# Optimization experiments

Hardware: AMD Instinct MI355X
Metric: run time of the kernel (lower is better)

Reference implementation:

```python
import jax, jax.numpy as jnp
import numpy as np

B, T, D_IN, H, D_DEC = 64, 512, 512, 1024, 1024


def _lstm_scan(xs, W_ih, W_hh, b_ih, b_hh):
    """xs: (T, B, D). Returns hs: (T, B, H), final (h, c). Zero initial state,
    matching torch.nn.LSTMCell default when no state is passed."""
    Bsz = xs.shape[1]
    Hsz = W_hh.shape[1]
    h0 = jnp.zeros((Bsz, Hsz), xs.dtype)
    c0 = jnp.zeros((Bsz, Hsz), xs.dtype)

    def step(carry, x):
        h, c = carry
        # gates: (B, 4H), torch order [i, f, g, o]
        g = x @ W_ih.T + b_ih + h @ W_hh.T + b_hh
        i, f, gg, o = jnp.split(g, 4, axis=-1)
        c_new = jax.nn.sigmoid(f) * c + jax.nn.sigmoid(i) * jnp.tanh(gg)
        h_new = jax.nn.sigmoid(o) * jnp.tanh(c_new)
        return (h_new, c_new), h_new

    (hT, cT), hs = jax.lax.scan(step, (h0, c0), xs)
    return hs, hT, cT


def setup_inputs() -> dict:
    key = jax.random.key(0)
    ks = jax.random.split(key, 14)
    s_cell = 1.0 / np.sqrt(H)
    s_fc = 1.0 / np.sqrt(2 * H)
    u = lambda k, shape, s: jax.random.uniform(k, shape, jnp.float32, -s, s)
    return {
        "embedding_input": jax.random.normal(ks[0], (B, T, D_IN), jnp.float32),
        "W_ih_f": u(ks[1], (4 * H, D_IN), s_cell),
        "W_hh_f": u(ks[2], (4 * H, H), s_cell),
        "b_ih_f": u(ks[3], (4 * H,), s_cell),
        "b_hh_f": u(ks[4], (4 * H,), s_cell),
        "W_ih_b": u(ks[5], (4 * H, D_IN), s_cell),
        "W_hh_b": u(ks[6], (4 * H, H), s_cell),
        "b_ih_b": u(ks[7], (4 * H,), s_cell),
        "b_hh_b": u(ks[8], (4 * H,), s_cell),
        "fc_W": u(ks[9], (D_DEC, 2 * H), s_fc),
        "fc_b": u(ks[10], (D_DEC,), s_fc),
        "fh_W": u(ks[11], (D_DEC, 2 * H), s_fc),
        "fh_b": u(ks[12], (D_DEC,), s_fc),
    }


def reference(embedding_input, W_ih_f, W_hh_f, b_ih_f, b_hh_f,
              W_ih_b, W_hh_b, b_ih_b, b_hh_b, fc_W, fc_b, fh_W, fh_b):
    xs = jnp.transpose(embedding_input, (1, 0, 2))  # (T, B, D)
    # forward direction over t = 0..T-1
    hs_f, hT_f, cT_f = _lstm_scan(xs, W_ih_f, W_hh_f, b_ih_f, b_hh_f)
    # backward direction over t = T-1..0; torch code stores these in
    # traversal order (NOT flipped back), so we keep that order.
    hs_b, hT_b, cT_b = _lstm_scan(xs[::-1], W_ih_b, W_hh_b, b_ih_b, b_hh_b)

    cell_end = jnp.concatenate([cT_f, cT_b], axis=-1)     # (B, 2H)
    hidden_end = jnp.concatenate([hT_f, hT_b], axis=-1)   # (B, 2H)
    initial_cells = jnp.tanh(cell_end @ fc_W.T + fc_b)
    initial_hiddens = jnp.tanh(hidden_end @ fh_W.T + fh_b)

    # (B, T, 2H): forward slot t = timestep t; backward slot t = timestep T-1-t
    hidden_states = jnp.concatenate([hs_f, hs_b], axis=-1).transpose(1, 0, 2)
    return hidden_states, (initial_hiddens, initial_cells)
```

## Files before the change

### kernel.cpp

```cpp
#include <hip/hip_runtime.h>
#include <stdint.h>
#include <math.h>


#define TSEQ 512
#define DIN  512

typedef short  short8  __attribute__((ext_vector_type(8)));
typedef float  float4_ __attribute__((ext_vector_type(4)));
typedef float  float8_ __attribute__((ext_vector_type(8)));

__device__ __forceinline__ unsigned short f2bf(float f) {
  union { float f; unsigned int i; } v; v.f = f;
  unsigned int r = (v.i + 0x7FFFu + ((v.i >> 16) & 1u)) >> 16;
  return (unsigned short)r;
}
__device__ __forceinline__ short8 cvt8(const float* p) {
  float8_ f = *reinterpret_cast<const float8_*>(p);
  short8 s;
  #pragma unroll
  for (int i = 0; i < 8; ++i) s[i] = (short)f2bf(f[i]);
  return s;
}
__device__ __forceinline__ short8 ald16(const unsigned long long* b64, size_t elem) {
  union { unsigned long long u[2]; short8 s; } v;
  const unsigned long long* p = b64 + (elem >> 2);
  v.u[0] = __hip_atomic_load(p,     __ATOMIC_RELAXED, __HIP_MEMORY_SCOPE_AGENT);
  v.u[1] = __hip_atomic_load(p + 1, __ATOMIC_RELAXED, __HIP_MEMORY_SCOPE_AGENT);
  return v.s;
}
__device__ __forceinline__ float sigf(float x) {
  x = fminf(fmaxf(x, -30.f), 30.f);
  return 1.f / (1.f + expf(-x));
}

__global__ __launch_bounds__(512, 2)
void lstm_encoder_kernel(
    const float* __restrict__ x,
    const float* __restrict__ Wih_f, const float* __restrict__ Whh_f,
    const float* __restrict__ bih_f, const float* __restrict__ bhh_f,
    const float* __restrict__ Wih_b, const float* __restrict__ Whh_b,
    const float* __restrict__ bih_b, const float* __restrict__ bhh_b,
    const float* __restrict__ fcW, const float* __restrict__ fcb,
    const float* __restrict__ fhW, const float* __restrict__ fhb,
    float* __restrict__ out,
    unsigned char* __restrict__ flags, int* __restrict__ done,
    unsigned short* __restrict__ hbuf_f, unsigned short* __restrict__ hbuf_b,
    unsigned short* __restrict__ cend)
{
  __shared__ float part[8][4][32][18];

  const int tid  = threadIdx.x;
  const int wv   = tid >> 6;
  const int lane = tid & 63;
  const int quad = lane >> 4;
  const int u16  = lane & 15;

  const int wg    = blockIdx.x;
  const int group = wg >> 7;
  const int rem   = wg & 127;
  const int dir   = rem >> 6;
  const int seg   = rem & 63;
  const int j0    = seg * 16;
  const int dom   = group * 2 + dir;
  unsigned char* myflags = flags + dom * 256;

  const float* Wih = dir ? Wih_b : Wih_f;
  const float* Whh = dir ? Whh_b : Whh_f;
  const float* bih = dir ? bih_b : bih_f;
  const float* bhh = dir ? bhh_b : bhh_f;
  unsigned short* hbuf = dir ? hbuf_b : hbuf_f;
  const unsigned long long* hbuf64 = (const unsigned long long*)hbuf;
  unsigned int* hbuf32 = (unsigned int*)hbuf;

  const int wx = wv * 64;
  const int wh = wv * 128;

  short8 Bf[6][4];
  #pragma unroll
  for (int kc = 0; kc < 6; ++kc) {
    #pragma unroll
    for (int nt = 0; nt < 4; ++nt) {
      const int row = nt * 1024 + j0 + u16;
      const float* p = (kc < 2)
          ? (Wih + (size_t)row * 512  + (wx + kc * 32 + quad * 8))
          : (Whh + (size_t)row * 1024 + (wh + (kc - 2) * 32 + quad * 8));
      Bf[kc][nt] = cvt8(p);
    }
  }
  float bias[4];
  #pragma unroll
  for (int g = 0; g < 4; ++g)
    bias[g] = bih[g * 1024 + j0 + u16] + bhh[g * 1024 + j0 + u16];

  float4_ acc[2][4];
  #pragma unroll
  for (int mt = 0; mt < 2; ++mt)
    #pragma unroll
    for (int nt = 0; nt < 4; ++nt) acc[mt][nt] = (float4_){0.f, 0.f, 0.f, 0.f};

  float cstate = 0.f;
  const int arow0 = group * 32 + u16;

  auto gemm_x = [&](int t) {
    const int tx = dir ? (TSEQ - 1 - t) : t;
    #pragma unroll
    for (int kc = 0; kc < 2; ++kc) {
      const int klane = wx + kc * 32 + quad * 8;
      const float* base = x + ((size_t)arow0 * TSEQ + tx) * DIN + klane;
      short8 a0 = cvt8(base);
      short8 a1 = cvt8(base + (size_t)16 * TSEQ * DIN);
      #pragma unroll
      for (int nt = 0; nt < 4; ++nt) {
        acc[0][nt] = __builtin_amdgcn_mfma_f32_16x16x32_bf16(a0, Bf[kc][nt], acc[0][nt], 0, 0, 0);
        acc[1][nt] = __builtin_amdgcn_mfma_f32_16x16x32_bf16(a1, Bf[kc][nt], acc[1][nt], 0, 0, 0);
      }
    }
  };
  auto gemm_h = [&](int t) {
    const int rp = (t + 1) & 1;
    #pragma unroll
    for (int kc = 2; kc < 6; ++kc) {
      const int kh = wh + (kc - 2) * 32 + quad * 8;
      const size_t eb = (size_t)(rp * 64 + arow0) * 1024 + kh;
      short8 a0 = ald16(hbuf64, eb);
      short8 a1 = ald16(hbuf64, eb + (size_t)16 * 1024);
      #pragma unroll
      for (int nt = 0; nt < 4; ++nt) {
        acc[0][nt] = __builtin_amdgcn_mfma_f32_16x16x32_bf16(a0, Bf[kc][nt], acc[0][nt], 0, 0, 0);
        acc[1][nt] = __builtin_amdgcn_mfma_f32_16x16x32_bf16(a1, Bf[kc][nt], acc[1][nt], 0, 0, 0);
      }
    }
  };

  gemm_x(0);

  const int row_l = wv * 4 + quad;
  const int bglob = group * 32 + row_l;

  for (int t = 0; t < TSEQ; ++t) {
    if (wv == 0) {
      const unsigned char tb = (unsigned char)t;
      int it = 0;
      for (;;) {
        unsigned char v = __hip_atomic_load(myflags + lane, __ATOMIC_RELAXED, __HIP_MEMORY_SCOPE_AGENT);
        if (__ballot((unsigned char)(v - tb) > 1u) == 0ull) break;
        if (++it > 300000) break;
        __builtin_amdgcn_s_sleep(2);
      }
    }
    __syncthreads();
    __builtin_amdgcn_fence(__ATOMIC_ACQUIRE, "workgroup");
    __builtin_amdgcn_sched_barrier(0);

    gemm_h(t);

    #pragma unroll
    for (int mt = 0; mt < 2; ++mt)
      #pragma unroll
      for (int nt = 0; nt < 4; ++nt)
        #pragma unroll
        for (int r = 0; r < 4; ++r)
          part[wv][nt][mt * 16 + quad * 4 + r][u16] = acc[mt][nt][r];
    __syncthreads();

    float gts[4];
    #pragma unroll
    for (int g = 0; g < 4; ++g) {
      float s = bias[g];
      #pragma unroll
      for (int p = 0; p < 8; ++p) s += part[p][g][row_l][u16];
      gts[g] = s;
    }
    float iv = sigf(gts[0]);
    float fv = sigf(gts[1]);
    float gv = tanhf(gts[2]);
    float ov = sigf(gts[3]);
    cstate = fv * cstate + iv * gv;
    float hv = ov * tanhf(cstate);
    unsigned short h16 = f2bf(hv);

    {
      unsigned int h32 = h16;
      unsigned int oth = __shfl_xor(h32, 1);
      if ((u16 & 1) == 0) {
        unsigned int val = h32 | (oth << 16);
        size_t elem = (size_t)((t & 1) * 64 + bglob) * 1024 + j0 + u16;
        __hip_atomic_store(hbuf32 + (elem >> 1), val, __ATOMIC_RELAXED, __HIP_MEMORY_SCOPE_AGENT);
      }
    }
    __syncthreads();

    if (tid == 0)
      __hip_atomic_store(myflags + seg, (unsigned char)(t + 1), __ATOMIC_RELAXED, __HIP_MEMORY_SCOPE_AGENT);

    #pragma unroll
    for (int mt = 0; mt < 2; ++mt)
      #pragma unroll
      for (int nt = 0; nt < 4; ++nt) acc[mt][nt] = (float4_){0.f, 0.f, 0.f, 0.f};
    if (t + 1 < TSEQ) gemm_x(t + 1);

    out[((size_t)bglob * TSEQ + t) * 2048 + dir * 1024 + j0 + u16] = hv;
  }

  {
    unsigned short c16 = f2bf(cstate);
    unsigned int c32 = c16;
    unsigned int oth = __shfl_xor(c32, 1);
    if ((u16 & 1) == 0) {
      size_t elem = (size_t)bglob * 2048 + dir * 1024 + j0 + u16;
      __hip_atomic_store((unsigned int*)cend + (elem >> 1), c32 | (oth << 16),
                         __ATOMIC_RELAXED, __HIP_MEMORY_SCOPE_AGENT);
    }
  }
  __syncthreads();
  if (tid == 0)
    __hip_atomic_store(done + wg, 1, __ATOMIC_RELAXED, __HIP_MEMORY_SCOPE_AGENT);
  if (wg >= 128) return;

  {
    int it = 0;
    for (;;) {
      int ok = 1;
      #pragma unroll
      for (int j = 0; j < 4; ++j) {
        int v = __hip_atomic_load(done + lane * 4 + j, __ATOMIC_RELAXED, __HIP_MEMORY_SCOPE_AGENT);
        ok &= (v != 0);
      }
      if (__ballot(!ok) == 0ull) break;
      if (++it > 300000) break;
      __builtin_amdgcn_s_sleep(4);
    }
    __builtin_amdgcn_fence(__ATOMIC_ACQUIRE, "workgroup");
    __builtin_amdgcn_sched_barrier(0);
  }
  if (wv >= 4) return;

  const int mat   = wg >> 6;
  const int nbase = (wg & 63) * 16;
  const float* Wp = mat ? fcW : fhW;
  const float* bp = mat ? fcb : fhb;
  const int m0 = wv * 16;
  const int am = m0 + u16;
  const unsigned long long* hf64 = (const unsigned long long*)hbuf_f;
  const unsigned long long* hb64 = (const unsigned long long*)hbuf_b;
  const unsigned long long* ce64 = (const unsigned long long*)cend;
  float4_ a4 = (float4_){0.f, 0.f, 0.f, 0.f};
  #pragma unroll 4
  for (int kc = 0; kc < 64; ++kc) {
    const int k = kc * 32 + quad * 8;
    short8 av, bv;
    if (mat == 0) {
      av = (kc < 32) ? ald16(hf64, (size_t)(64 + am) * 1024 + k)
                     : ald16(hb64, (size_t)(64 + am) * 1024 + (k - 1024));
    } else {
      av = ald16(ce64, (size_t)am * 2048 + k);
    }
    bv = cvt8(Wp + (size_t)(nbase + u16) * 2048 + k);
    a4 = __builtin_amdgcn_mfma_f32_16x16x32_bf16(av, bv, a4, 0, 0, 0);
  }
  float bb = bp[nbase + u16];
  #pragma unroll
  for (int r = 0; r < 4; ++r) {
    const int row = m0 + quad * 4 + r;
    float v = tanhf(a4[r] + bb);
    out[(size_t)67108864 + (size_t)mat * 65536 + (size_t)row * 1024 + nbase + u16] = v;
  }
}

extern "C" void kernel_launch(void* const* d_in, const int* in_sizes, int n_in,
                              void* d_out, int out_size, void* d_ws, size_t ws_size,
                              hipStream_t stream) {
  char* ws = (char*)d_ws;
  unsigned char* flags = (unsigned char*)(ws);
  int* done  = (int*)(ws + 4096);
  unsigned short* hf = (unsigned short*)(ws + 8192);
  unsigned short* hb = (unsigned short*)(ws + 8192 + 262144);
  unsigned short* ce = (unsigned short*)(ws + 8192 + 524288);
  hipMemsetAsync(d_ws, 0, 8192 + 524288, stream);
  lstm_encoder_kernel<<<256, 512, 0, stream>>>(
      (const float*)d_in[0],
      (const float*)d_in[1], (const float*)d_in[2],
      (const float*)d_in[3], (const float*)d_in[4],
      (const float*)d_in[5], (const float*)d_in[6],
      (const float*)d_in[7], (const float*)d_in[8],
      (const float*)d_in[9], (const float*)d_in[10],
      (const float*)d_in[11], (const float*)d_in[12],
      (float*)d_out, flags, done, hf, hb, ce);
}
```

Baseline: 4.094 ms.

## Replace per-step flag polling with sentinel-valued h buffers and 4-slot ring

Result: no change. 4.101 ms (+0.2%).

```diff
diff --git a/kernel.cpp b/kernel.cpp
--- a/kernel.cpp
+++ b/kernel.cpp
@@ -44,7 +44,7 @@
     const float* __restrict__ fcW, const float* __restrict__ fcb,
     const float* __restrict__ fhW, const float* __restrict__ fhb,
     float* __restrict__ out,
-    unsigned char* __restrict__ flags, int* __restrict__ done,
+    int* __restrict__ done,
     unsigned short* __restrict__ hbuf_f, unsigned short* __restrict__ hbuf_b,
     unsigned short* __restrict__ cend)
 {
@@ -62,8 +62,6 @@
   const int dir   = rem >> 6;
   const int seg   = rem & 63;
   const int j0    = seg * 16;
-  const int dom   = group * 2 + dir;
-  unsigned char* myflags = flags + dom * 256;
 
   const float* Wih = dir ? Wih_b : Wih_f;
   const float* Whh = dir ? Whh_b : Whh_f;
@@ -117,18 +115,47 @@
       }
     }
   };
+
   auto gemm_h = [&](int t) {
-    const int rp = (t + 1) & 1;
-    #pragma unroll
-    for (int kc = 2; kc < 6; ++kc) {
-      const int kh = wh + (kc - 2) * 32 + quad * 8;
-      const size_t eb = (size_t)(rp * 64 + arow0) * 1024 + kh;
-      short8 a0 = ald16(hbuf64, eb);
-      short8 a1 = ald16(hbuf64, eb + (size_t)16 * 1024);
+    const int rp = (t + 3) & 3;
+    const unsigned long long* base[4];
+    #pragma unroll
+    for (int kc = 0; kc < 4; ++kc) {
+      const int kh = wh + kc * 32 + quad * 8;
+      base[kc] = hbuf64 + ((((size_t)(rp * 64 + arow0)) * 1024 + kh) >> 2);
+    }
+    unsigned long long v[4][4];
+    int it = 0;
+    for (;;) {
+      #pragma unroll
+      for (int kc = 0; kc < 4; ++kc) {
+        v[kc][0] = __hip_atomic_load(base[kc],        __ATOMIC_RELAXED, __HIP_MEMORY_SCOPE_AGENT);
+        v[kc][1] = __hip_atomic_load(base[kc] + 1,    __ATOMIC_RELAXED, __HIP_MEMORY_SCOPE_AGENT);
+        v[kc][2] = __hip_atomic_load(base[kc] + 4096, __ATOMIC_RELAXED, __HIP_MEMORY_SCOPE_AGENT);
+        v[kc][3] = __hip_atomic_load(base[kc] + 4097, __ATOMIC_RELAXED, __HIP_MEMORY_SCOPE_AGENT);
+      }
+      unsigned long long bad = 0;
+      #pragma unroll
+      for (int kc = 0; kc < 4; ++kc)
+        #pragma unroll
+        for (int j = 0; j < 4; ++j) {
+          unsigned long long y = ~v[kc][j];
+          bad |= (y - 0x0001000100010001ull) & ~y & 0x8000800080008000ull;
+        }
+      if (__ballot(bad != 0) == 0ull) break;
+      if (++it > 200000) break;
+      if (it < 4) __builtin_amdgcn_s_sleep(1);
+      else        __builtin_amdgcn_s_sleep(4);
+    }
+    #pragma unroll
+    for (int kc = 0; kc < 4; ++kc) {
+      union { unsigned long long u[2]; short8 s; } a0, a1;
+      a0.u[0] = v[kc][0]; a0.u[1] = v[kc][1];
+      a1.u[0] = v[kc][2]; a1.u[1] = v[kc][3];
       #pragma unroll
       for (int nt = 0; nt < 4; ++nt) {
-        acc[0][nt] = __builtin_amdgcn_mfma_f32_16x16x32_bf16(a0, Bf[kc][nt], acc[0][nt], 0, 0, 0);
-        acc[1][nt] = __builtin_amdgcn_mfma_f32_16x16x32_bf16(a1, Bf[kc][nt], acc[1][nt], 0, 0, 0);
+        acc[0][nt] = __builtin_amdgcn_mfma_f32_16x16x32_bf16(a0.s, Bf[kc + 2][nt], acc[0][nt], 0, 0, 0);
+        acc[1][nt] = __builtin_amdgcn_mfma_f32_16x16x32_bf16(a1.s, Bf[kc + 2][nt], acc[1][nt], 0, 0, 0);
       }
     }
   };
@@ -139,19 +166,16 @@
   const int bglob = group * 32 + row_l;
 
   for (int t = 0; t < TSEQ; ++t) {
-    if (wv == 0) {
-      const unsigned char tb = (unsigned char)t;
-      int it = 0;
-      for (;;) {
-        unsigned char v = __hip_atomic_load(myflags + lane, __ATOMIC_RELAXED, __HIP_MEMORY_SCOPE_AGENT);
-        if (__ballot((unsigned char)(v - tb) > 1u) == 0ull) break;
-        if (++it > 300000) break;
-        __builtin_amdgcn_s_sleep(2);
-      }
-    }
-    __syncthreads();
-    __builtin_amdgcn_fence(__ATOMIC_ACQUIRE, "workgroup");
-    __builtin_amdgcn_sched_barrier(0);
+    {
+      const int rq = (t + 1) & 3;
+      if (tid < 256) {
+        const int rr = group * 32 + (tid >> 3);
+        const int uu = j0 + ((tid & 7) << 1);
+        const size_t elem = (size_t)(rq * 64 + rr) * 1024 + uu;
+        __hip_atomic_store(hbuf32 + (elem >> 1), 0xFFFFFFFFu,
+                           __ATOMIC_RELAXED, __HIP_MEMORY_SCOPE_AGENT);
+      }
+    }
 
     gemm_h(t);
 
@@ -185,22 +209,23 @@
       unsigned int oth = __shfl_xor(h32, 1);
       if ((u16 & 1) == 0) {
         unsigned int val = h32 | (oth << 16);
-        size_t elem = (size_t)((t & 1) * 64 + bglob) * 1024 + j0 + u16;
-        __hip_atomic_store(hbuf32 + (elem >> 1), val, __ATOMIC_RELAXED, __HIP_MEMORY_SCOPE_AGENT);
-      }
-    }
-    __syncthreads();
-
-    if (tid == 0)
-      __hip_atomic_store(myflags + seg, (unsigned char)(t + 1), __ATOMIC_RELAXED, __HIP_MEMORY_SCOPE_AGENT);
+        size_t elem = (size_t)((t & 3) * 64 + bglob) * 1024 + j0 + u16;
+        __hip_atomic_store(hbuf32 + (elem >> 1), val,
+                           __ATOMIC_RELAXED, __HIP_MEMORY_SCOPE_AGENT);
+      }
+    }
+
+    asm volatile("s_waitcnt lgkmcnt(0)" ::: "memory");
+    __builtin_amdgcn_s_barrier();
+    __builtin_amdgcn_sched_barrier(0);
+
+    out[((size_t)bglob * TSEQ + t) * 2048 + dir * 1024 + j0 + u16] = hv;
 
     #pragma unroll
     for (int mt = 0; mt < 2; ++mt)
       #pragma unroll
       for (int nt = 0; nt < 4; ++nt) acc[mt][nt] = (float4_){0.f, 0.f, 0.f, 0.f};
     if (t + 1 < TSEQ) gemm_x(t + 1);
-
-    out[((size_t)bglob * TSEQ + t) * 2048 + dir * 1024 + j0 + u16] = hv;
   }
 
   {
@@ -251,8 +276,8 @@
     const int k = kc * 32 + quad * 8;
     short8 av, bv;
     if (mat == 0) {
-      av = (kc < 32) ? ald16(hf64, (size_t)(64 + am) * 1024 + k)
-                     : ald16(hb64, (size_t)(64 + am) * 1024 + (k - 1024));
+      av = (kc < 32) ? ald16(hf64, (size_t)(192 + am) * 1024 + k)
+                     : ald16(hb64, (size_t)(192 + am) * 1024 + (k - 1024));
     } else {
       av = ald16(ce64, (size_t)am * 2048 + k);
     }
@@ -272,12 +297,15 @@
                               void* d_out, int out_size, void* d_ws, size_t ws_size,
                               hipStream_t stream) {
   char* ws = (char*)d_ws;
-  unsigned char* flags = (unsigned char*)(ws);
-  int* done  = (int*)(ws + 4096);
-  unsigned short* hf = (unsigned short*)(ws + 8192);
-  unsigned short* hb = (unsigned short*)(ws + 8192 + 262144);
-  unsigned short* ce = (unsigned short*)(ws + 8192 + 524288);
-  hipMemsetAsync(d_ws, 0, 8192 + 524288, stream);
+  int* done = (int*)(ws);
+  unsigned short* hf = (unsigned short*)(ws + 4096);
+  unsigned short* hb = (unsigned short*)(ws + 4096 + 524288);
+  unsigned short* ce = (unsigned short*)(ws + 4096 + 1048576);
+  (void)hipMemsetAsync(ws, 0, 4096, stream);
+  (void)hipMemsetAsync(hf, 0xFF, 393216, stream);
+  (void)hipMemsetAsync((char*)hf + 393216, 0, 131072, stream);
+  (void)hipMemsetAsync(hb, 0xFF, 393216, stream);
+  (void)hipMemsetAsync((char*)hb + 393216, 0, 131072, stream);
   lstm_encoder_kernel<<<256, 512, 0, stream>>>(
       (const float*)d_in[0],
       (const float*)d_in[1], (const float*)d_in[2],
@@ -286,5 +314,5 @@
       (const float*)d_in[7], (const float*)d_in[8],
       (const float*)d_in[9], (const float*)d_in[10],
       (const float*)d_in[11], (const float*)d_in[12],
-      (float*)d_out, flags, done, hf, hb, ce);
-}
+      (float*)d_out, done, hf, hb, ce);
+}
```
